# Performance work log

Hardware: AMD Instinct MI355X
Metric: run time of the kernel (lower is better)

Reference implementation:

```python
import jax, jax.numpy as jnp
import numpy as np

N = 100000  # nodes


def _gcn_conv(x, W, b, src, dst, dis, n):
    # GCNConv: linear transform first (out_dim small), then normalized aggregate
    h = x @ W                                   # [N, out]
    norm = dis[src] * dis[dst]                  # [E']
    msg = norm[:, None] * h[src]                # [E', out]
    out = jax.ops.segment_sum(msg, dst, num_segments=n)
    return out + b


def setup_inputs() -> dict:
    key = jax.random.key(0)
    ks = jax.random.split(key, 4)
    F_IN, HID, C, E = 512, 16, 16, 3200000
    x = jax.random.normal(ks[0], (N, F_IN), dtype=jnp.float32)
    edge_index = jax.random.randint(ks[1], (2, E), 0, N, dtype=jnp.int32)
    W1 = jax.random.normal(ks[2], (F_IN, HID), dtype=jnp.float32) * (1.0 / np.sqrt(F_IN))
    b1 = jnp.zeros((HID,), dtype=jnp.float32)
    W2 = jax.random.normal(ks[3], (HID, C), dtype=jnp.float32) * (1.0 / np.sqrt(HID))
    b2 = jnp.zeros((C,), dtype=jnp.float32)
    return {"x": x, "edge_index": edge_index, "W1": W1, "b1": b1, "W2": W2, "b2": b2}


def reference(x, edge_index, W1, b1, W2, b2):
    n = x.shape[0]
    loop = jnp.arange(n, dtype=edge_index.dtype)
    src = jnp.concatenate([edge_index[0], loop])  # add self-loops (GCNConv default)
    dst = jnp.concatenate([edge_index[1], loop])
    deg = jax.ops.segment_sum(jnp.ones_like(dst, dtype=x.dtype), dst, num_segments=n)
    dis = jnp.where(deg > 0, jax.lax.rsqrt(deg), 0.0)  # deg^{-1/2}
    # dropout is identity in eval mode
    h = jax.nn.elu(_gcn_conv(x, W1, b1, src, dst, dis, n))
    out = _gcn_conv(h, W2, b2, src, dst, dis, n)
    return jax.nn.log_softmax(out, axis=1)
```

## Files before the change

### kernel.cpp

```cpp
#include <hip/hip_runtime.h>

#define TPB 256
#define BKT_SHIFT 8
#define BKT_SZ 256
#define CHUNK 8192

__global__ void k_count(const int* __restrict__ dst, int* __restrict__ counts,
                        int E, int NB, int NCHUNK) {
  __shared__ int hist[512];
  int t = threadIdx.x;
  for (int d = t; d < NB; d += TPB) hist[d] = 0;
  __syncthreads();
  int base = blockIdx.x * CHUNK;
  for (int i = t; i < CHUNK; i += TPB) {
    int e = base + i;
    if (e < E) atomicAdd(&hist[dst[e] >> BKT_SHIFT], 1);
  }
  __syncthreads();
  for (int d = t; d < NB; d += TPB)
    counts[d * NCHUNK + blockIdx.x] = hist[d];
}

__global__ void k_scan1(int* __restrict__ a, int* __restrict__ btot, int total) {
  __shared__ int s[TPB];
  int t = threadIdx.x;
  int i = blockIdx.x * TPB + t;
  int v = (i < total) ? a[i] : 0;
  s[t] = v;
  __syncthreads();
  for (int d = 1; d < TPB; d <<= 1) {
    int u = (t >= d) ? s[t - d] : 0;
    __syncthreads();
    s[t] += u;
    __syncthreads();
  }
  if (i < total) a[i] = s[t] - v;
  if (t == TPB - 1) btot[blockIdx.x] = s[t];
}

__global__ void k_scan2(int* __restrict__ btot, int nb) {
  __shared__ int s[1024];
  int t = threadIdx.x;
  int v = (t < nb) ? btot[t] : 0;
  s[t] = v;
  __syncthreads();
  for (int d = 1; d < 1024; d <<= 1) {
    int u = (t >= d) ? s[t - d] : 0;
    __syncthreads();
    s[t] += u;
    __syncthreads();
  }
  if (t < nb) btot[t] = s[t] - v;
}

__global__ void k_part(const int* __restrict__ src, const int* __restrict__ dst,
                       const int* __restrict__ cnts, const int* __restrict__ btot,
                       unsigned int* __restrict__ part, int E, int NB, int NCHUNK) {
  __shared__ int cur[512];
  int t = threadIdx.x;
  for (int d = t; d < NB; d += TPB) {
    int idx = d * NCHUNK + blockIdx.x;
    cur[d] = cnts[idx] + btot[idx >> 8];
  }
  __syncthreads();
  int base = blockIdx.x * CHUNK;
  for (int i = t; i < CHUNK; i += TPB) {
    int e = base + i;
    if (e < E) {
      int dv = dst[e];
      int d = dv >> BKT_SHIFT;
      int p = atomicAdd(&cur[d], 1);
      part[p] = ((unsigned)src[e] << BKT_SHIFT) | (unsigned)(dv & (BKT_SZ - 1));
    }
  }
}

__global__ __launch_bounds__(256) void k_build(
    const unsigned int* __restrict__ part, const int* __restrict__ cnts,
    const int* __restrict__ btot,
    int* __restrict__ offs, int* __restrict__ csr, float* __restrict__ dis,
    int n, int E, int NB, int NCHUNK) {
  __shared__ int cnt[BKT_SZ];
  __shared__ int scn[BKT_SZ];
  int b = blockIdx.x, t = threadIdx.x;
  cnt[t] = 0;
  __syncthreads();
  int i0 = b * NCHUNK;
  int beg = cnts[i0] + btot[i0 >> 8];
  int end = E;
  if (b + 1 < NB) {
    int i1 = (b + 1) * NCHUNK;
    end = cnts[i1] + btot[i1 >> 8];
  }
  for (int e = beg + t; e < end; e += 256)
    atomicAdd(&cnt[part[e] & (BKT_SZ - 1)], 1);
  __syncthreads();
  int deg = cnt[t];
  scn[t] = deg;
  __syncthreads();
  for (int d = 1; d < 256; d <<= 1) {
    int u = (t >= d) ? scn[t - d] : 0;
    __syncthreads();
    scn[t] += u;
    __syncthreads();
  }
  int excl = scn[t] - deg;
  int node = b * BKT_SZ + t;
  if (node < n) {
    offs[node] = beg + excl;
    dis[node] = 1.0f / sqrtf((float)(deg + 1));
  }
  if (b == NB - 1 && t == 0) offs[n] = E;
  __syncthreads();
  cnt[t] = beg + excl;
  __syncthreads();
  for (int e = beg + t; e < end; e += 256) {
    unsigned int en = part[e];
    int p = atomicAdd(&cnt[en & (BKT_SZ - 1)], 1);
    csr[p] = (int)(en >> BKT_SHIFT);
  }
}

__global__ __launch_bounds__(256) void k_gemm1(
    const float* __restrict__ x, const float* __restrict__ W1,
    const float* __restrict__ dis, float* __restrict__ hs, int n, int nwaves) {
  const int lane = threadIdx.x & 63;
  const int wave = blockIdx.x * 4 + (threadIdx.x >> 6);

  float w[8][16];
  #pragma unroll
  for (int m = 0; m < 8; ++m) {
    #pragma unroll
    for (int q = 0; q < 4; ++q) {
      float4 t = *reinterpret_cast<const float4*>(W1 + (lane * 8 + m) * 16 + q * 4);
      w[m][q * 4 + 0] = t.x; w[m][q * 4 + 1] = t.y;
      w[m][q * 4 + 2] = t.z; w[m][q * 4 + 3] = t.w;
    }
  }
  const int c_out = ((lane & 1) << 3) | ((lane & 2) << 1) | ((lane & 4) >> 1) | ((lane & 8) >> 3);

  float4 a = {0, 0, 0, 0}, b = {0, 0, 0, 0};
  if (wave < n) {
    const float4* xp = reinterpret_cast<const float4*>(x + (size_t)wave * 512);
    a = xp[lane * 2]; b = xp[lane * 2 + 1];
  }

  for (int i = wave; i < n; ) {
    int inext = i + nwaves;
    float4 an = {0, 0, 0, 0}, bn = {0, 0, 0, 0};
    if (inext < n) {
      const float4* xp = reinterpret_cast<const float4*>(x + (size_t)inext * 512);
      an = xp[lane * 2]; bn = xp[lane * 2 + 1];
    }

    float xv[8] = {a.x, a.y, a.z, a.w, b.x, b.y, b.z, b.w};
    float acc[16];
    #pragma unroll
    for (int c = 0; c < 16; ++c) acc[c] = 0.f;
    #pragma unroll
    for (int m = 0; m < 8; ++m) {
      #pragma unroll
      for (int c = 0; c < 16; ++c) acc[c] = fmaf(xv[m], w[m][c], acc[c]);
    }

    {
      const bool hi = (lane & 1) != 0;
      #pragma unroll
      for (int v = 0; v < 8; ++v) {
        float send = hi ? acc[v] : acc[v + 8];
        float rcv = __shfl_xor(send, 1);
        acc[v] = (hi ? acc[v + 8] : acc[v]) + rcv;
      }
    }
    {
      const bool hi = (lane & 2) != 0;
      #pragma unroll
      for (int v = 0; v < 4; ++v) {
        float send = hi ? acc[v] : acc[v + 4];
        float rcv = __shfl_xor(send, 2);
        acc[v] = (hi ? acc[v + 4] : acc[v]) + rcv;
      }
    }
    {
      const bool hi = (lane & 4) != 0;
      #pragma unroll
      for (int v = 0; v < 2; ++v) {
        float send = hi ? acc[v] : acc[v + 2];
        float rcv = __shfl_xor(send, 4);
        acc[v] = (hi ? acc[v + 2] : acc[v]) + rcv;
      }
    }
    {
      const bool hi = (lane & 8) != 0;
      float send = hi ? acc[0] : acc[1];
      float rcv = __shfl_xor(send, 8);
      acc[0] = (hi ? acc[1] : acc[0]) + rcv;
    }
    float vsum = acc[0];
    vsum += __shfl_xor(vsum, 16);
    vsum += __shfl_xor(vsum, 32);

    if (lane < 16) hs[(size_t)i * 16 + c_out] = dis[i] * vsum;

    a = an; b = bn; i = inext;
  }
}

__global__ __launch_bounds__(256) void k_agg1(
    const int* __restrict__ offs, const int* __restrict__ csr,
    const float* __restrict__ hs, const float* __restrict__ dis,
    const float* __restrict__ b1, float* __restrict__ h1s, int n) {
  int wave = blockIdx.x * 4 + (threadIdx.x >> 6);
  if (wave >= n) return;
  int lane = threadIdx.x & 63;
  int c4 = lane & 3, r = lane >> 2;
  int beg = offs[wave], end = offs[wave + 1];
  const float4* hs4 = reinterpret_cast<const float4*>(hs);

  float ax = 0.f, ay = 0.f, az = 0.f, aw = 0.f;
  int k = beg + r;
  int s = (k < end) ? csr[k] : 0;
  while (k < end) {
    int k2 = k + 16;
    int s2 = (k2 < end) ? csr[k2] : 0;
    float4 v = hs4[(size_t)s * 4 + c4];
    ax += v.x; ay += v.y; az += v.z; aw += v.w;
    s = s2; k = k2;
  }
  #pragma unroll
  for (int m = 4; m <= 32; m <<= 1) {
    ax += __shfl_xor(ax, m); ay += __shfl_xor(ay, m);
    az += __shfl_xor(az, m); aw += __shfl_xor(aw, m);
  }
  float4 sf = hs4[(size_t)wave * 4 + c4];
  float di = dis[wave];
  float4 b1v = reinterpret_cast<const float4*>(b1)[c4];
  float ox = fmaf(di, ax + sf.x, b1v.x);
  float oy = fmaf(di, ay + sf.y, b1v.y);
  float oz = fmaf(di, az + sf.z, b1v.z);
  float ow = fmaf(di, aw + sf.w, b1v.w);
  float4 o;
  o.x = di * (ox > 0.f ? ox : expm1f(ox));
  o.y = di * (oy > 0.f ? oy : expm1f(oy));
  o.z = di * (oz > 0.f ? oz : expm1f(oz));
  o.w = di * (ow > 0.f ? ow : expm1f(ow));
  if (r == 0) reinterpret_cast<float4*>(h1s)[(size_t)wave * 4 + c4] = o;
}

__global__ __launch_bounds__(256) void k_agg2(
    const int* __restrict__ offs, const int* __restrict__ csr,
    const float* __restrict__ h1s, const float* __restrict__ dis,
    const float* __restrict__ W2, const float* __restrict__ b2,
    float* __restrict__ out, int n) {
  __shared__ float w2s[256];
  w2s[threadIdx.x] = W2[threadIdx.x];
  __syncthreads();
  int wave = blockIdx.x * 4 + (threadIdx.x >> 6);
  if (wave >= n) return;
  int lane = threadIdx.x & 63;
  int c4 = lane & 3, r = lane >> 2;
  int beg = offs[wave], end = offs[wave + 1];
  const float4* h4 = reinterpret_cast<const float4*>(h1s);

  float ax = 0.f, ay = 0.f, az = 0.f, aw = 0.f;
  int k = beg + r;
  int s = (k < end) ? csr[k] : 0;
  while (k < end) {
    int k2 = k + 16;
    int s2 = (k2 < end) ? csr[k2] : 0;
    float4 v = h4[(size_t)s * 4 + c4];
    ax += v.x; ay += v.y; az += v.z; aw += v.w;
    s = s2; k = k2;
  }
  #pragma unroll
  for (int m = 4; m <= 32; m <<= 1) {
    ax += __shfl_xor(ax, m); ay += __shfl_xor(ay, m);
    az += __shfl_xor(az, m); aw += __shfl_xor(aw, m);
  }
  float4 sf = h4[(size_t)wave * 4 + c4];
  float di = dis[wave];
  float sx = di * (ax + sf.x);
  float sy = di * (ay + sf.y);
  float sz = di * (az + sf.z);
  float sw = di * (aw + sf.w);
  int c = lane & 15;
  int lbase = lane & ~3;
  float dot = 0.f;
  #pragma unroll
  for (int k16 = 0; k16 < 16; ++k16) {
    int srcl = lbase | (k16 >> 2);
    float comp = (k16 & 3) == 0 ? sx : (k16 & 3) == 1 ? sy : (k16 & 3) == 2 ? sz : sw;
    float vk = __shfl(comp, srcl);
    dot = fmaf(vk, w2s[k16 * 16 + c], dot);
  }
  float o = dot + b2[c];
  float m = o;
  m = fmaxf(m, __shfl_xor(m, 1));
  m = fmaxf(m, __shfl_xor(m, 2));
  m = fmaxf(m, __shfl_xor(m, 4));
  m = fmaxf(m, __shfl_xor(m, 8));
  float ex = expf(o - m);
  float ssum = ex;
  ssum += __shfl_xor(ssum, 1);
  ssum += __shfl_xor(ssum, 2);
  ssum += __shfl_xor(ssum, 4);
  ssum += __shfl_xor(ssum, 8);
  if (lane < 16) out[(size_t)wave * 16 + c] = o - m - logf(ssum);
}

extern "C" void kernel_launch(void* const* d_in, const int* in_sizes, int n_in,
                              void* d_out, int out_size, void* d_ws, size_t ws_size,
                              hipStream_t stream) {
  const float* x  = (const float*)d_in[0];
  const int*   ei = (const int*)d_in[1];
  const float* W1 = (const float*)d_in[2];
  const float* b1 = (const float*)d_in[3];
  const float* W2 = (const float*)d_in[4];
  const float* b2 = (const float*)d_in[5];
  float* out = (float*)d_out;

  const int n = in_sizes[0] / 512;
  const int E = in_sizes[1] / 2;
  const int* src = ei;
  const int* dst = ei + E;

  const int NB = (n + BKT_SZ - 1) >> BKT_SHIFT;
  const int NCHUNK = (E + CHUNK - 1) / CHUNK;
  const int total = NB * NCHUNK;
  const int sb = (total + TPB - 1) / TPB;

  char* ws = (char*)d_ws;
  size_t off = 0;
  auto alloc = [&](size_t bytes) -> void* {
    void* p = (void*)(ws + off);
    off += (bytes + 255) & ~(size_t)255;
    return p;
  };
  int*          counts = (int*)alloc((size_t)total * 4);
  int*          btot   = (int*)alloc(1024 * 4);
  unsigned int* part   = (unsigned int*)alloc((size_t)E * 4);
  int*          offs   = (int*)alloc((size_t)(n + 1) * 4);
  int*          csr    = (int*)alloc((size_t)E * 4);
  float*        dis    = (float*)alloc((size_t)n * 4);
  float*        hs     = (float*)alloc((size_t)n * 16 * 4);
  float*        h1s    = (float*)alloc((size_t)n * 16 * 4);
  (void)ws_size; (void)n_in; (void)out_size;

  const int ab = (n + 3) / 4;

  k_count<<<NCHUNK, TPB, 0, stream>>>(dst, counts, E, NB, NCHUNK);
  k_scan1<<<sb, TPB, 0, stream>>>(counts, btot, total);
  k_scan2<<<1, 1024, 0, stream>>>(btot, sb);
  k_part <<<NCHUNK, TPB, 0, stream>>>(src, dst, counts, btot, part, E, NB, NCHUNK);
  k_build<<<NB, TPB, 0, stream>>>(part, counts, btot, offs, csr, dis, n, E, NB, NCHUNK);
  k_gemm1<<<2048, TPB, 0, stream>>>(x, W1, dis, hs, n, 2048 * 4);
  k_agg1 <<<ab, TPB, 0, stream>>>(offs, csr, hs, dis, b1, h1s, n);
  k_agg2 <<<ab, TPB, 0, stream>>>(offs, csr, h1s, dis, W2, b2, out, n);
}
```

Before: 543.8 us.

## Fuse count and partition into one pass using fixed-capacity buckets

```diff
diff --git a/kernel.cpp b/kernel.cpp
--- a/kernel.cpp
+++ b/kernel.cpp
@@ -4,94 +4,46 @@
 #define BKT_SHIFT 8
 #define BKT_SZ 256
 #define CHUNK 8192
-
-__global__ void k_count(const int* __restrict__ dst, int* __restrict__ counts,
-                        int E, int NB, int NCHUNK) {
+#define BKT_STRIDE 16384
+
+__global__ void k_countpart(const int* __restrict__ src, const int* __restrict__ dst,
+                            int* __restrict__ gcur, unsigned int* __restrict__ part,
+                            int E, int NB) {
   __shared__ int hist[512];
+  __shared__ int cur[512];
   int t = threadIdx.x;
   for (int d = t; d < NB; d += TPB) hist[d] = 0;
   __syncthreads();
   int base = blockIdx.x * CHUNK;
-  for (int i = t; i < CHUNK; i += TPB) {
-    int e = base + i;
-    if (e < E) atomicAdd(&hist[dst[e] >> BKT_SHIFT], 1);
-  }
-  __syncthreads();
-  for (int d = t; d < NB; d += TPB)
-    counts[d * NCHUNK + blockIdx.x] = hist[d];
-}
-
-__global__ void k_scan1(int* __restrict__ a, int* __restrict__ btot, int total) {
-  __shared__ int s[TPB];
-  int t = threadIdx.x;
-  int i = blockIdx.x * TPB + t;
-  int v = (i < total) ? a[i] : 0;
-  s[t] = v;
-  __syncthreads();
-  for (int d = 1; d < TPB; d <<= 1) {
-    int u = (t >= d) ? s[t - d] : 0;
-    __syncthreads();
-    s[t] += u;
-    __syncthreads();
-  }
-  if (i < total) a[i] = s[t] - v;
-  if (t == TPB - 1) btot[blockIdx.x] = s[t];
-}
-
-__global__ void k_scan2(int* __restrict__ btot, int nb) {
-  __shared__ int s[1024];
-  int t = threadIdx.x;
-  int v = (t < nb) ? btot[t] : 0;
-  s[t] = v;
-  __syncthreads();
-  for (int d = 1; d < 1024; d <<= 1) {
-    int u = (t >= d) ? s[t - d] : 0;
-    __syncthreads();
-    s[t] += u;
-    __syncthreads();
-  }
-  if (t < nb) btot[t] = s[t] - v;
-}
-
-__global__ void k_part(const int* __restrict__ src, const int* __restrict__ dst,
-                       const int* __restrict__ cnts, const int* __restrict__ btot,
-                       unsigned int* __restrict__ part, int E, int NB, int NCHUNK) {
-  __shared__ int cur[512];
-  int t = threadIdx.x;
+  int lim = min(base + CHUNK, E);
+  for (int e = base + t; e < lim; e += TPB)
+    atomicAdd(&hist[dst[e] >> BKT_SHIFT], 1);
+  __syncthreads();
   for (int d = t; d < NB; d += TPB) {
-    int idx = d * NCHUNK + blockIdx.x;
-    cur[d] = cnts[idx] + btot[idx >> 8];
-  }
-  __syncthreads();
-  int base = blockIdx.x * CHUNK;
-  for (int i = t; i < CHUNK; i += TPB) {
-    int e = base + i;
-    if (e < E) {
-      int dv = dst[e];
-      int d = dv >> BKT_SHIFT;
-      int p = atomicAdd(&cur[d], 1);
-      part[p] = ((unsigned)src[e] << BKT_SHIFT) | (unsigned)(dv & (BKT_SZ - 1));
-    }
+    int h = hist[d];
+    int b = h ? atomicAdd(&gcur[d], h) : 0;
+    cur[d] = d * BKT_STRIDE + b;
+  }
+  __syncthreads();
+  for (int e = base + t; e < lim; e += TPB) {
+    int dv = dst[e];
+    int d = dv >> BKT_SHIFT;
+    int p = atomicAdd(&cur[d], 1);
+    part[p] = ((unsigned)src[e] << BKT_SHIFT) | (unsigned)(dv & (BKT_SZ - 1));
   }
 }
 
 __global__ __launch_bounds__(256) void k_build(
-    const unsigned int* __restrict__ part, const int* __restrict__ cnts,
-    const int* __restrict__ btot,
-    int* __restrict__ offs, int* __restrict__ csr, float* __restrict__ dis,
-    int n, int E, int NB, int NCHUNK) {
+    const unsigned int* __restrict__ part, const int* __restrict__ gcur,
+    int* __restrict__ offs, int* __restrict__ degs, int* __restrict__ csr,
+    float* __restrict__ dis, int n, int NB) {
   __shared__ int cnt[BKT_SZ];
   __shared__ int scn[BKT_SZ];
   int b = blockIdx.x, t = threadIdx.x;
   cnt[t] = 0;
   __syncthreads();
-  int i0 = b * NCHUNK;
-  int beg = cnts[i0] + btot[i0 >> 8];
-  int end = E;
-  if (b + 1 < NB) {
-    int i1 = (b + 1) * NCHUNK;
-    end = cnts[i1] + btot[i1 >> 8];
-  }
+  int beg = b * BKT_STRIDE;
+  int end = beg + gcur[b];
   for (int e = beg + t; e < end; e += 256)
     atomicAdd(&cnt[part[e] & (BKT_SZ - 1)], 1);
   __syncthreads();
@@ -108,9 +60,9 @@
   int node = b * BKT_SZ + t;
   if (node < n) {
     offs[node] = beg + excl;
+    degs[node] = deg;
     dis[node] = 1.0f / sqrtf((float)(deg + 1));
   }
-  if (b == NB - 1 && t == 0) offs[n] = E;
   __syncthreads();
   cnt[t] = beg + excl;
   __syncthreads();
@@ -207,14 +159,15 @@
 }
 
 __global__ __launch_bounds__(256) void k_agg1(
-    const int* __restrict__ offs, const int* __restrict__ csr,
+    const int* __restrict__ offs, const int* __restrict__ degs,
+    const int* __restrict__ csr,
     const float* __restrict__ hs, const float* __restrict__ dis,
     const float* __restrict__ b1, float* __restrict__ h1s, int n) {
   int wave = blockIdx.x * 4 + (threadIdx.x >> 6);
   if (wave >= n) return;
   int lane = threadIdx.x & 63;
   int c4 = lane & 3, r = lane >> 2;
-  int beg = offs[wave], end = offs[wave + 1];
+  int beg = offs[wave], end = beg + degs[wave];
   const float4* hs4 = reinterpret_cast<const float4*>(hs);
 
   float ax = 0.f, ay = 0.f, az = 0.f, aw = 0.f;
@@ -248,7 +201,8 @@
 }
 
 __global__ __launch_bounds__(256) void k_agg2(
-    const int* __restrict__ offs, const int* __restrict__ csr,
+    const int* __restrict__ offs, const int* __restrict__ degs,
+    const int* __restrict__ csr,
     const float* __restrict__ h1s, const float* __restrict__ dis,
     const float* __restrict__ W2, const float* __restrict__ b2,
     float* __restrict__ out, int n) {
@@ -259,7 +213,7 @@
   if (wave >= n) return;
   int lane = threadIdx.x & 63;
   int c4 = lane & 3, r = lane >> 2;
-  int beg = offs[wave], end = offs[wave + 1];
+  int beg = offs[wave], end = beg + degs[wave];
   const float4* h4 = reinterpret_cast<const float4*>(h1s);
 
   float ax = 0.f, ay = 0.f, az = 0.f, aw = 0.f;
@@ -326,8 +280,6 @@
 
   const int NB = (n + BKT_SZ - 1) >> BKT_SHIFT;
   const int NCHUNK = (E + CHUNK - 1) / CHUNK;
-  const int total = NB * NCHUNK;
-  const int sb = (total + TPB - 1) / TPB;
 
   char* ws = (char*)d_ws;
   size_t off = 0;
@@ -336,24 +288,22 @@
     off += (bytes + 255) & ~(size_t)255;
     return p;
   };
-  int*          counts = (int*)alloc((size_t)total * 4);
-  int*          btot   = (int*)alloc(1024 * 4);
-  unsigned int* part   = (unsigned int*)alloc((size_t)E * 4);
-  int*          offs   = (int*)alloc((size_t)(n + 1) * 4);
-  int*          csr    = (int*)alloc((size_t)E * 4);
-  float*        dis    = (float*)alloc((size_t)n * 4);
-  float*        hs     = (float*)alloc((size_t)n * 16 * 4);
-  float*        h1s    = (float*)alloc((size_t)n * 16 * 4);
+  int*          gcur = (int*)alloc((size_t)NB * 4);
+  unsigned int* part = (unsigned int*)alloc((size_t)NB * BKT_STRIDE * 4);
+  int*          offs = (int*)alloc((size_t)n * 4);
+  int*          degs = (int*)alloc((size_t)n * 4);
+  int*          csr  = (int*)alloc((size_t)NB * BKT_STRIDE * 4);
+  float*        dis  = (float*)alloc((size_t)n * 4);
+  float*        hs   = (float*)alloc((size_t)n * 16 * 4);
+  float*        h1s  = (float*)alloc((size_t)n * 16 * 4);
   (void)ws_size; (void)n_in; (void)out_size;
 
   const int ab = (n + 3) / 4;
 
-  k_count<<<NCHUNK, TPB, 0, stream>>>(dst, counts, E, NB, NCHUNK);
-  k_scan1<<<sb, TPB, 0, stream>>>(counts, btot, total);
-  k_scan2<<<1, 1024, 0, stream>>>(btot, sb);
-  k_part <<<NCHUNK, TPB, 0, stream>>>(src, dst, counts, btot, part, E, NB, NCHUNK);
-  k_build<<<NB, TPB, 0, stream>>>(part, counts, btot, offs, csr, dis, n, E, NB, NCHUNK);
-  k_gemm1<<<2048, TPB, 0, stream>>>(x, W1, dis, hs, n, 2048 * 4);
-  k_agg1 <<<ab, TPB, 0, stream>>>(offs, csr, hs, dis, b1, h1s, n);
-  k_agg2 <<<ab, TPB, 0, stream>>>(offs, csr, h1s, dis, W2, b2, out, n);
-}
+  hipMemsetAsync(gcur, 0, (size_t)NB * 4, stream);
+  k_countpart<<<NCHUNK, TPB, 0, stream>>>(src, dst, gcur, part, E, NB);
+  k_build    <<<NB, TPB, 0, stream>>>(part, gcur, offs, degs, csr, dis, n, NB);
+  k_gemm1    <<<2048, TPB, 0, stream>>>(x, W1, dis, hs, n, 2048 * 4);
+  k_agg1     <<<ab, TPB, 0, stream>>>(offs, degs, csr, hs, dis, b1, h1s, n);
+  k_agg2     <<<ab, TPB, 0, stream>>>(offs, degs, csr, h1s, dis, W2, b2, out, n);
+}
```

Measured after the change: 546.0 us. About the same (+0.4%).
